# Optimization experiments

Hardware: AMD Instinct MI355X
Metric: run time of the kernel (lower is better)

Reference implementation:

```python
import jax, jax.numpy as jnp
import numpy as np

GRID = 128  # voxel grid extent
N_PTS = 100000


def _hash(c):
    c = c.astype(np.int64) + 16  # shift so offset-perturbed coords stay non-negative
    return (c[:, 0] * 512 + c[:, 1]) * 512 + c[:, 2]


def _offsets(vals):
    v = np.asarray(vals)
    return np.stack(np.meshgrid(v, v, v, indexing='ij'), axis=-1).reshape(-1, 3)


def _build_kmap(cin, cout, offsets):
    # For each kernel offset o, find pairs (in_idx, out_idx) with coord_in == coord_out + o.
    ki = _hash(cin)
    order = np.argsort(ki)
    ks = ki[order]
    ins, outs = [], []
    for o in offsets:
        q = _hash(cout + o[None, :])
        pos = np.searchsorted(ks, q)
        pc = np.clip(pos, 0, len(ks) - 1)
        found = ks[pc] == q
        ins.append(order[pc[found]])
        outs.append(np.nonzero(found)[0])
    K = len(offsets)
    P = max(1, max(len(a) for a in ins))
    in_idx = np.full((K, P), len(cin), np.int32)   # pad -> zero row of padded feats
    out_idx = np.full((K, P), len(cout), np.int32)  # pad -> dummy output row
    for k in range(K):
        in_idx[k, :len(ins[k])] = ins[k]
        out_idx[k, :len(outs[k])] = outs[k]
    return in_idx, out_idx


def _conv(x, W, in_idx, out_idx, n_out):
    # Minkowski sparse conv: per kernel offset, gather -> matmul -> scatter-add.
    xp = jnp.concatenate([x, jnp.zeros((1, x.shape[1]), x.dtype)], axis=0)
    out0 = jnp.zeros((n_out + 1, W.shape[-1]), x.dtype)

    def step(acc, kio):
        Wk, ik, ok = kio
        return acc.at[ok].add(xp[ik] @ Wk), None

    out, _ = jax.lax.scan(step, out0, (W, in_idx, out_idx))
    return out[:n_out]


def _bn(x, gamma, beta, eps=1e-5):
    # training-mode batch norm over the point dimension (biased variance)
    m = jnp.mean(x, axis=0)
    v = jnp.mean((x - m) ** 2, axis=0)
    return (x - m) * jax.lax.rsqrt(v + eps) * gamma + beta


def _forward(feats, W0, g0, b0,
             Ws1, gs1, bs1, Wa1, ga1, ba1, Wb1, gb1, bb1,
             Ws2, gs2, bs2, Wa2, ga2, ba2, Wb2, gb2, bb2, Wd2, gd2, bd2,
             Ws3, gs3, bs3, Wa3, ga3, ba3, Wb3, gb3, bb3, Wd3, gd3, bd3,
             c1, c2, c3,
             im0, om0, ims1, oms1, imb1, omb1, ims2, oms2, imb2, omb2,
             ims3, oms3, imb3, omb3):
    relu = jax.nn.relu
    n0, n1, n2, n3 = feats.shape[0], c1.shape[0], c2.shape[0], c3.shape[0]
    # stem: 5x5x5 conv + BN + ReLU (output coords == input coords)
    x = relu(_bn(_conv(feats, W0, im0, om0, n0), g0, b0))
    # level 1: stride-2 conv + BN + ReLU, then BasicBlock 64->64 (identity residual)
    x = relu(_bn(_conv(x, Ws1, ims1, oms1, n1), gs1, bs1))
    h = relu(_bn(_conv(x, Wa1, imb1, omb1, n1), ga1, ba1))
    h = _bn(_conv(h, Wb1, imb1, omb1, n1), gb1, bb1)
    y1 = relu(h + x)
    # level 2: stride-2 conv, then BasicBlock 64->128 (1x1 conv + BN residual)
    x = relu(_bn(_conv(y1, Ws2, ims2, oms2, n2), gs2, bs2))
    res = _bn(x @ Wd2, gd2, bd2)
    h = relu(_bn(_conv(x, Wa2, imb2, omb2, n2), ga2, ba2))
    h = _bn(_conv(h, Wb2, imb2, omb2, n2), gb2, bb2)
    y2 = relu(h + res)
    # level 3: stride-2 conv, then BasicBlock 128->256 (1x1 conv + BN residual)
    x = relu(_bn(_conv(y2, Ws3, ims3, oms3, n3), gs3, bs3))
    res = _bn(x @ Wd3, gd3, bd3)
    h = relu(_bn(_conv(x, Wa3, imb3, omb3, n3), ga3, ba3))
    h = _bn(_conv(h, Wb3, imb3, omb3, n3), gb3, bb3)
    y3 = relu(h + res)
    return (y1, y2, y3)


def setup_inputs() -> dict:
    rng = np.random.default_rng(0)
    c0 = np.unique(rng.integers(0, GRID, size=(N_PTS, 3)), axis=0).astype(np.int32)
    c1 = np.unique(c0 // 2 * 2, axis=0)
    c2 = np.unique(c1 // 4 * 4, axis=0)
    c3 = np.unique(c2 // 8 * 8, axis=0)
    im0, om0 = _build_kmap(c0, c0, _offsets([-2, -1, 0, 1, 2]))  # conv0 k=5, ts=1
    ims1, oms1 = _build_kmap(c0, c1, _offsets([0, 1]))           # stride-2, ts_in=1
    imb1, omb1 = _build_kmap(c1, c1, _offsets([-2, 0, 2]))       # k=3 at ts=2
    ims2, oms2 = _build_kmap(c1, c2, _offsets([0, 2]))
    imb2, omb2 = _build_kmap(c2, c2, _offsets([-4, 0, 4]))       # k=3 at ts=4
    ims3, oms3 = _build_kmap(c2, c3, _offsets([0, 4]))
    imb3, omb3 = _build_kmap(c3, c3, _offsets([-8, 0, 8]))       # k=3 at ts=8
    keys = iter(jax.random.split(jax.random.key(0), 16))

    def kai3(K, ci, co):  # kaiming_normal fan_out for [K, Cin, Cout] sparse kernels
        return jax.random.normal(next(keys), (K, ci, co), jnp.float32) * np.float32(np.sqrt(2.0 / (K * co)))

    def kai2(ci, co):
        return jax.random.normal(next(keys), (ci, co), jnp.float32) * np.float32(np.sqrt(2.0 / co))

    ones = lambda c: jnp.ones((c,), jnp.float32)
    zeros = lambda c: jnp.zeros((c,), jnp.float32)
    feats = jax.random.normal(next(keys), (c0.shape[0], 1), jnp.float32)
    return dict(
        feats=feats,
        W0=kai3(125, 1, 64), g0=ones(64), b0=zeros(64),
        Ws1=kai3(8, 64, 64), gs1=ones(64), bs1=zeros(64),
        Wa1=kai3(27, 64, 64), ga1=ones(64), ba1=zeros(64),
        Wb1=kai3(27, 64, 64), gb1=ones(64), bb1=zeros(64),
        Ws2=kai3(8, 64, 64), gs2=ones(64), bs2=zeros(64),
        Wa2=kai3(27, 64, 128), ga2=ones(128), ba2=zeros(128),
        Wb2=kai3(27, 128, 128), gb2=ones(128), bb2=zeros(128),
        Wd2=kai2(64, 128), gd2=ones(128), bd2=zeros(128),
        Ws3=kai3(8, 128, 128), gs3=ones(128), bs3=zeros(128),
        Wa3=kai3(27, 128, 256), ga3=ones(256), ba3=zeros(256),
        Wb3=kai3(27, 256, 256), gb3=ones(256), bb3=zeros(256),
        Wd3=kai2(128, 256), gd3=ones(256), bd3=zeros(256),
        c1=jnp.asarray(c1), c2=jnp.asarray(c2), c3=jnp.asarray(c3),
        im0=jnp.asarray(im0), om0=jnp.asarray(om0),
        ims1=jnp.asarray(ims1), oms1=jnp.asarray(oms1),
        imb1=jnp.asarray(imb1), omb1=jnp.asarray(omb1),
        ims2=jnp.asarray(ims2), oms2=jnp.asarray(oms2),
        imb2=jnp.asarray(imb2), omb2=jnp.asarray(omb2),
        ims3=jnp.asarray(ims3), oms3=jnp.asarray(oms3),
        imb3=jnp.asarray(imb3), omb3=jnp.asarray(omb3),
    )


def reference(feats, W0, g0, b0,
              Ws1, gs1, bs1, Wa1, ga1, ba1, Wb1, gb1, bb1,
              Ws2, gs2, bs2, Wa2, ga2, ba2, Wb2, gb2, bb2, Wd2, gd2, bd2,
              Ws3, gs3, bs3, Wa3, ga3, ba3, Wb3, gb3, bb3, Wd3, gd3, bd3,
              c1, c2, c3,
              im0, om0, ims1, oms1, imb1, omb1, ims2, oms2, imb2, omb2,
              ims3, oms3, imb3, omb3):
    return _forward(feats, W0, g0, b0,
                    Ws1, gs1, bs1, Wa1, ga1, ba1, Wb1, gb1, bb1,
                    Ws2, gs2, bs2, Wa2, ga2, ba2, Wb2, gb2, bb2, Wd2, gd2, bd2,
                    Ws3, gs3, bs3, Wa3, ga3, ba3, Wb3, gb3, bb3, Wd3, gd3, bd3,
                    c1, c2, c3,
                    im0, om0, ims1, oms1, imb1, omb1, ims2, oms2, imb2, omb2,
                    ims3, oms3, imb3, omb3)
```

## Files before the change

kernel.cpp:

```cpp
#include <hip/hip_runtime.h>
#include <hip/hip_bf16.h>
#include <cstdint>
#include <cstddef>

typedef __attribute__((ext_vector_type(8))) short sh8;
typedef __attribute__((ext_vector_type(4))) short sh4;
typedef __attribute__((ext_vector_type(4))) int ix4;
typedef __attribute__((ext_vector_type(16))) float floatx16;
typedef unsigned short ushort_t;

__device__ __forceinline__ void glds16(const ushort_t* g, ushort_t* l) {
  __builtin_amdgcn_global_load_lds(
      (const __attribute__((address_space(1))) void*)g,
      (__attribute__((address_space(3))) void*)l, 16, 0, 0);
}

__device__ __forceinline__ ushort_t f2bf_bits(float f) {
  __hip_bfloat16 b = __float2bfloat16(f);
  return __builtin_bit_cast(unsigned short, b);
}

__global__ void build_ell_kernel(const int* __restrict__ in_idx,
                                 const int* __restrict__ out_idx,
                                 int K, int S, int P, int n_in, int n_out,
                                 int* __restrict__ ell) {
  int i = blockIdx.x * 256 + threadIdx.x;
  if (i >= K * P) return;
  int vin = in_idx[i];
  int vout = out_idx[i];
  if (vin < n_in && vout < n_out) {
    ell[(size_t)vout * S + (i / P)] = vin;
  }
}

__global__ void pack_u_kernel(const float* __restrict__ W,
                              __hip_bfloat16* __restrict__ Wp,
                              int K, int CSPLIT, int COUT, long total) {
  long i = (long)blockIdx.x * 256 + threadIdx.x;
  if (i >= total) return;
  int co = (int)(i % COUT);
  long t = i / COUT;
  int vch = (int)(t % 64);
  int vk = (int)(t / 64);
  int k = vk / CSPLIT;
  int ci = (vk % CSPLIT) * 64 + vch;
  int CIN = CSPLIT * 64;
  float v = (k < K) ? W[((long)k * CIN + ci) * COUT + co] : 0.f;
  Wp[(((long)vk * 8 + (vch >> 3)) * COUT + co) * 8 + (vch & 7)] =
      __float2bfloat16(v);
}

__global__ void pack_w0_kernel(const float* __restrict__ W,
                               __hip_bfloat16* __restrict__ Wp) {
  int i = blockIdx.x * 256 + threadIdx.x;
  if (i >= 128 * 64) return;
  int co = i & 63;
  int ki = i >> 6;
  float v = (ki < 125) ? W[ki * 64 + co] : 0.f;
  Wp[(((ki >> 4) * 64) + co) * 16 + (ki & 15)] = __float2bfloat16(v);
}

__global__ void f2bf_kernel(const float* __restrict__ x,
                            __hip_bfloat16* __restrict__ y, long n, long npad) {
  long i = (long)blockIdx.x * 256 + threadIdx.x;
  if (i >= npad) return;
  y[i] = __float2bfloat16(i < n ? x[i] : 0.f);
}

__global__ void reduce_parts_kernel(const float* __restrict__ part, int P,
                                    long total, float* __restrict__ out) {
  long i = (long)blockIdx.x * 256 + threadIdx.x;
  if (i >= total) return;
  float s = 0.f;
  for (int p = 0; p < P; ++p) s += part[(size_t)p * total + i];
  out[i] = s;
}

__global__ __launch_bounds__(256, 2) void conv0_mfma_kernel(
    const ushort_t* __restrict__ xpad, const ushort_t* __restrict__ Wp0,
    const int* __restrict__ ell, int n_out, float* __restrict__ out) {
  constexpr int STR = 152;
  __shared__ ushort_t xs[64 * STR];
  const int tid = threadIdx.x;
  const int lane = tid & 63;
  const int wv = tid >> 6;
  const int wm = wv & 1, wn = wv >> 1;
  const long m0 = (long)blockIdx.x * 64;
  const int row = tid >> 2;
  const int kk0 = (tid & 3) * 32;
  const long grow = m0 + row;

  if (grow < n_out) {
    const ix4* ep = (const ix4*)(ell + grow * 128 + kk0);
#pragma unroll
    for (int g = 0; g < 8; ++g) {
      ix4 e = ep[g];
      sh4 v;
#pragma unroll
      for (int j = 0; j < 4; ++j) {
        int ix = (e[j] < 0) ? n_out : e[j];
        v[j] = (short)xpad[ix];
      }
      *(sh4*)(&xs[row * STR + kk0 + g * 4]) = v;
    }
  } else {
    sh4 z = (sh4)(short)0;
#pragma unroll
    for (int g = 0; g < 8; ++g) *(sh4*)(&xs[row * STR + kk0 + g * 4]) = z;
  }
  __syncthreads();

  const int arow = wm * 32 + (lane & 31);
  const int koff = (lane >> 5) * 8;
  const int bcol = wn * 32 + (lane & 31);
  floatx16 acc = (floatx16)(0.0f);
#pragma unroll
  for (int kc = 0; kc < 8; ++kc) {
    sh8 a = *(const sh8*)(&xs[arow * STR + kc * 16 + koff]);
    sh8 b = *(const sh8*)(Wp0 + ((size_t)kc * 64 + bcol) * 16 + koff);
    acc = __builtin_amdgcn_mfma_f32_32x32x16_bf16(a, b, acc, 0, 0, 0);
  }
  const int lrow = (lane >> 5) * 4;
#pragma unroll
  for (int r = 0; r < 16; ++r) {
    long orow = m0 + wm * 32 + (r & 3) + 8 * (r >> 2) + lrow;
    if (orow < n_out) out[orow * 64 + bcol] = acc[r];
  }
}

template <int CSPLIT, int CT>
__global__ __launch_bounds__(CT * 4, CT == 128 ? 4 : 2) void conv_u_kernel(
    const ushort_t* __restrict__ xb, const ushort_t* __restrict__ Wp,
    const int* __restrict__ ell, int S, int KI, int KP, int kdense,
    int n_out, int n_in, int COfull, int MB, int KS, int CS,
    float* __restrict__ out) {
  constexpr int BLK = CT * 4;
  constexpr int NWN = CT / 32;
  constexpr int ASEG_PW = 16 / (BLK / 64);
  constexpr int BSEG_PW = (CT / 8) / (BLK / 64);
  constexpr int RW = CSPLIT * 64;
  __shared__ ushort_t Ab[2][128 * 64];
  __shared__ ushort_t Bb[2][8 * CT * 8];
  __shared__ int ells[128 * 28];
  const int tid = threadIdx.x;
  const int lane = tid & 63;
  const int wv = tid >> 6;
  const int wm = wv / NWN, wn = wv % NWN;

  const int total = MB * KS * CS;
  const int l = blockIdx.x;
  const int q = total >> 3, r8 = total & 7;
  const int xcd = l & 7, pos = l >> 3;
  const int lp = (xcd < r8) ? (xcd * (q + 1) + pos)
                            : (r8 * (q + 1) + (xcd - r8) * q + pos);
  const int mblk = lp / (KS * CS);
  const int rem = lp - mblk * (KS * CS);
  const int yk = rem / CS;
  const int zc = rem - yk * CS;
  const long m0 = (long)mblk * 128;
  const int colbase = zc * CT;

  for (int idx = tid; idx < 128 * S; idx += BLK) {
    int r = idx / S, k = idx - r * S;
    long grow = m0 + r;
    int v = -1;
    if (grow < n_out) {
      if (ell) v = ell[grow * (long)S + k];
      else if (k < kdense) v = (int)grow;
    }
    ells[idx] = (v < 0) ? n_in : v;
  }
  __syncthreads();

  const int i0 = yk * KP;
  int cnt = KI - i0;
  if (cnt > KP) cnt = KP;
  out += (size_t)yk * ((size_t)n_out * COfull);

  floatx16 acc0 = (floatx16)(0.0f);
  floatx16 acc1 = (floatx16)(0.0f);

  auto stage = [&](int vk, ushort_t* A, ushort_t* B) {
    const int sub = (CSPLIT == 1) ? 0 : (vk % CSPLIT);
    const int kq = (CSPLIT == 1) ? vk : (vk / CSPLIT);
#pragma unroll
    for (int i = 0; i < ASEG_PW; ++i) {
      const int s = wv * ASEG_PW + i;
      const int r = s * 8 + (lane >> 3);
      const int c = lane & 7;
      const int lc = c ^ (r & 7);
      const int e = ells[r * S + kq];
      glds16(xb + (size_t)e * RW + sub * 64 + lc * 8, A + s * 512 + lane * 8);
    }
    const ushort_t* wb = Wp + (size_t)vk * 8 * COfull * 8;
#pragma unroll
    for (int i = 0; i < BSEG_PW; ++i) {
      const int s = wv * BSEG_PW + i;
      int lc, co;
      if (CT == 128) { lc = s >> 1; co = (s & 1) * 64 + lane; }
      else           { lc = s;      co = lane; }
      glds16(wb + ((size_t)lc * COfull + colbase + co) * 8,
             B + s * 512 + lane * 8);
    }
  };
  auto compute = [&](const ushort_t* A, const ushort_t* B) {
    const int r0 = wm * 64 + (lane & 31);
    const int h = lane >> 5;
    const int co = wn * 32 + (lane & 31);
#pragma unroll
    for (int kc = 0; kc < 4; ++kc) {
      const int lc = kc * 2 + h;
      const int pc = lc ^ (r0 & 7);
      sh8 a0 = *(const sh8*)(A + r0 * 64 + pc * 8);
      sh8 a1 = *(const sh8*)(A + (r0 + 32) * 64 + pc * 8);
      sh8 b = *(const sh8*)(B + ((size_t)lc * CT + co) * 8);
      acc0 = __builtin_amdgcn_mfma_f32_32x32x16_bf16(a0, b, acc0, 0, 0, 0);
      acc1 = __builtin_amdgcn_mfma_f32_32x32x16_bf16(a1, b, acc1, 0, 0, 0);
    }
  };

  stage(i0, Ab[0], Bb[0]);

#define CONV_ITER(J, P)                                                        \
  if ((J) < cnt) {                                                             \
    __builtin_amdgcn_s_barrier();                                              \
    if ((J) + 1 < cnt) {                                                       \
      stage(i0 + (J) + 1, Ab[(P) ^ 1], Bb[(P) ^ 1]);                           \
      if constexpr (CT == 128)                                                 \
        asm volatile("s_waitcnt vmcnt(4)" ::: "memory");                       \
      else                                                                     \
        asm volatile("s_waitcnt vmcnt(6)" ::: "memory");                       \
    } else {                                                                   \
      asm volatile("s_waitcnt vmcnt(0)" ::: "memory");                         \
    }                                                                          \
    __builtin_amdgcn_s_barrier();                                              \
    __builtin_amdgcn_sched_barrier(0);                                         \
    compute(Ab[P], Bb[P]);                                                     \
  }

  for (int j = 0; j < cnt; j += 2) {
    CONV_ITER(j, 0)
    CONV_ITER(j + 1, 1)
  }
#undef CONV_ITER

  const int ccol = colbase + wn * 32 + (lane & 31);
  const int rb = wm * 64 + (lane >> 5) * 4;
#pragma unroll
  for (int rr = 0; rr < 16; ++rr) {
    long row = m0 + rb + (rr & 3) + 8 * (rr >> 2);
    if (row < n_out) out[row * COfull + ccol] = acc0[rr];
    long row1 = row + 32;
    if (row1 < n_out) out[row1 * COfull + ccol] = acc1[rr];
  }
}

template <int C>
__global__ void bn_reduce1_kernel(const float* __restrict__ x, int n,
                                  float* __restrict__ part) {
  constexpr int C4 = C / 4;
  constexpr int RL = 256 / C4;
  const int c4 = threadIdx.x % C4;
  const int rl = threadIdx.x / C4;
  float4 s = {0.f, 0.f, 0.f, 0.f}, ss = {0.f, 0.f, 0.f, 0.f};
  for (long row = (long)blockIdx.x * RL + rl; row < n;
       row += (long)gridDim.x * RL) {
    float4 v = *(const float4*)(x + row * C + c4 * 4);
    s.x += v.x; s.y += v.y; s.z += v.z; s.w += v.w;
    ss.x += v.x * v.x; ss.y += v.y * v.y; ss.z += v.z * v.z; ss.w += v.w * v.w;
  }
  __shared__ float4 sh[512];
  sh[threadIdx.x] = s;
  sh[256 + threadIdx.x] = ss;
  __syncthreads();
  if (rl == 0) {
#pragma unroll
    for (int j = 1; j < RL; ++j) {
      float4 a = sh[j * C4 + c4];
      float4 b = sh[256 + j * C4 + c4];
      s.x += a.x; s.y += a.y; s.z += a.z; s.w += a.w;
      ss.x += b.x; ss.y += b.y; ss.z += b.z; ss.w += b.w;
    }
    *(float4*)(part + (size_t)blockIdx.x * 2 * C + c4 * 4) = s;
    *(float4*)(part + (size_t)blockIdx.x * 2 * C + C + c4 * 4) = ss;
  }
}

template <int C>
__global__ void bn_reduce2_kernel(const float* __restrict__ part, int G,
                                  float* __restrict__ stats) {
  const int c = blockIdx.x;
  const int g = threadIdx.x;
  __shared__ float sh[512];
  float s = 0.f, ss = 0.f;
  if (g < G) {
    s = part[(size_t)g * 2 * C + c];
    ss = part[(size_t)g * 2 * C + C + c];
  }
  sh[g] = s;
  sh[256 + g] = ss;
  __syncthreads();
#pragma unroll
  for (int off = 128; off > 0; off >>= 1) {
    if (g < off) {
      sh[g] += sh[g + off];
      sh[256 + g] += sh[256 + g + off];
    }
    __syncthreads();
  }
  if (g == 0) {
    stats[c] = sh[0];
    stats[C + c] = sh[256];
  }
}

template <int C, bool RELU, bool RES, bool WF32>
__global__ void bn_apply_kernel(const float* __restrict__ x,
                                const float* __restrict__ stats,
                                const float* __restrict__ gamma,
                                const float* __restrict__ beta,
                                const float* __restrict__ res,
                                long total4, float inv_n,
                                float* __restrict__ out,
                                ushort_t* __restrict__ outb, long padEnd4) {
  constexpr int C4 = C / 4;
  for (long i = (long)blockIdx.x * 256 + threadIdx.x; i < padEnd4;
       i += (long)gridDim.x * 256) {
    if (i >= total4) {
      if (outb) *(ushort4*)(outb + i * 4) = (ushort4){0, 0, 0, 0};
      continue;
    }
    const int c4 = (int)(i % C4);
    float4 sum = *(const float4*)(stats + c4 * 4);
    float4 sq = *(const float4*)(stats + C + c4 * 4);
    float4 g4 = *(const float4*)(gamma + c4 * 4);
    float4 b4 = *(const float4*)(beta + c4 * 4);
    float4 v = *(const float4*)(x + i * 4);
    float4 r4 = {0.f, 0.f, 0.f, 0.f};
    if (RES) r4 = *(const float4*)(res + i * 4);
    float o[4];
#pragma unroll
    for (int j = 0; j < 4; ++j) {
      float m = ((const float*)&sum)[j] * inv_n;
      float var = ((const float*)&sq)[j] * inv_n - m * m;
      float sc = rsqrtf(var + 1e-5f) * ((const float*)&g4)[j];
      float val = (((const float*)&v)[j] - m) * sc + ((const float*)&b4)[j];
      if (RES) val += ((const float*)&r4)[j];
      if (RELU) val = fmaxf(val, 0.f);
      o[j] = val;
    }
    if (WF32) *(float4*)(out + i * 4) = (float4){o[0], o[1], o[2], o[3]};
    if (outb) {
      ushort4 w = {f2bf_bits(o[0]), f2bf_bits(o[1]), f2bf_bits(o[2]),
                   f2bf_bits(o[3])};
      *(ushort4*)(outb + i * 4) = w;
    }
  }
}


extern "C" void kernel_launch(void* const* d_in, const int* in_sizes, int n_in,
                              void* d_out, int out_size, void* d_ws,
                              size_t ws_size, hipStream_t stream) {
  const float* feats = (const float*)d_in[0];
  const float* W0  = (const float*)d_in[1];
  const float* g0  = (const float*)d_in[2];
  const float* b0  = (const float*)d_in[3];
  const float* Ws1 = (const float*)d_in[4];
  const float* gs1 = (const float*)d_in[5];
  const float* bs1 = (const float*)d_in[6];
  const float* Wa1 = (const float*)d_in[7];
  const float* ga1 = (const float*)d_in[8];
  const float* ba1 = (const float*)d_in[9];
  const float* Wb1 = (const float*)d_in[10];
  const float* gb1 = (const float*)d_in[11];
  const float* bb1 = (const float*)d_in[12];
  const float* Ws2 = (const float*)d_in[13];
  const float* gs2 = (const float*)d_in[14];
  const float* bs2 = (const float*)d_in[15];
  const float* Wa2 = (const float*)d_in[16];
  const float* ga2 = (const float*)d_in[17];
  const float* ba2 = (const float*)d_in[18];
  const float* Wb2 = (const float*)d_in[19];
  const float* gb2 = (const float*)d_in[20];
  const float* bb2 = (const float*)d_in[21];
  const float* Wd2 = (const float*)d_in[22];
  const float* gd2 = (const float*)d_in[23];
  const float* bd2 = (const float*)d_in[24];
  const float* Ws3 = (const float*)d_in[25];
  const float* gs3 = (const float*)d_in[26];
  const float* bs3 = (const float*)d_in[27];
  const float* Wa3 = (const float*)d_in[28];
  const float* ga3 = (const float*)d_in[29];
  const float* ba3 = (const float*)d_in[30];
  const float* Wb3 = (const float*)d_in[31];
  const float* gb3 = (const float*)d_in[32];
  const float* bb3 = (const float*)d_in[33];
  const float* Wd3 = (const float*)d_in[34];
  const float* gd3 = (const float*)d_in[35];
  const float* bd3 = (const float*)d_in[36];
  const int* im0  = (const int*)d_in[40];
  const int* om0  = (const int*)d_in[41];
  const int* ims1 = (const int*)d_in[42];
  const int* oms1 = (const int*)d_in[43];
  const int* imb1 = (const int*)d_in[44];
  const int* omb1 = (const int*)d_in[45];
  const int* ims2 = (const int*)d_in[46];
  const int* oms2 = (const int*)d_in[47];
  const int* imb2 = (const int*)d_in[48];
  const int* omb2 = (const int*)d_in[49];
  const int* ims3 = (const int*)d_in[50];
  const int* oms3 = (const int*)d_in[51];
  const int* imb3 = (const int*)d_in[52];
  const int* omb3 = (const int*)d_in[53];

  const int n0 = in_sizes[0];
  const int n1 = in_sizes[37] / 3;
  const int n2 = in_sizes[38] / 3;
  const int n3 = in_sizes[39] / 3;
  const int P0  = in_sizes[40] / 125;
  const int Ps1 = in_sizes[42] / 8;
  const int Pb1 = in_sizes[44] / 27;
  const int Ps2 = in_sizes[46] / 8;
  const int Pb2 = in_sizes[48] / 27;
  const int Ps3 = in_sizes[50] / 8;
  const int Pb3 = in_sizes[52] / 27;

  char* w = (char*)d_ws;
  auto carve = [&](size_t bytes) {
    char* p = w;
    w += (bytes + 255) & ~(size_t)255;
    return p;
  };
  int* ellS = (int*)carve((size_t)n0 * 128 * sizeof(int));
  int* ellB = (int*)carve((size_t)n1 * 28 * sizeof(int));
  float* part = (float*)carve((size_t)256 * 512 * sizeof(float));
  float* stats = (float*)carve((size_t)512 * sizeof(float));
  size_t capE = (size_t)n0 * 64 + 512;
  float* buf1 = (float*)carve(capE * sizeof(float));
  float* buf2 = (float*)carve(capE * sizeof(float));
  float* buf3 = (float*)carve(capE * sizeof(float));
  __hip_bfloat16* bbA = (__hip_bfloat16*)carve(capE * 2);
  __hip_bfloat16* bbB = (__hip_bfloat16*)carve(capE * 2);
  __hip_bfloat16* bbC = (__hip_bfloat16*)carve(capE * 2);
  __hip_bfloat16* xfeat = (__hip_bfloat16*)carve(((size_t)n0 + 1) * 2);

  auto packu = [&](const float* W, int K, int cin, int cout) {
    int csplit = cin / 64;
    long tot = (long)K * csplit * 64 * cout;
    __hip_bfloat16* Wp = (__hip_bfloat16*)carve((size_t)tot * 2);
    pack_u_kernel<<<(int)((tot + 255) / 256), 256, 0, stream>>>(
        W, Wp, K, csplit, cout, tot);
    return Wp;
  };
  __hip_bfloat16* Wp0 = (__hip_bfloat16*)carve((size_t)128 * 64 * 2);
  pack_w0_kernel<<<32, 256, 0, stream>>>(W0, Wp0);
  __hip_bfloat16* Ps1p = packu(Ws1, 8, 64, 64);
  __hip_bfloat16* Pa1p = packu(Wa1, 27, 64, 64);
  __hip_bfloat16* Pb1p = packu(Wb1, 27, 64, 64);
  __hip_bfloat16* Ps2p = packu(Ws2, 8, 64, 64);
  __hip_bfloat16* Pd2p = packu(Wd2, 1, 64, 128);
  __hip_bfloat16* Pa2p = packu(Wa2, 27, 64, 128);
  __hip_bfloat16* Pb2p = packu(Wb2, 27, 128, 128);
  __hip_bfloat16* Ps3p = packu(Ws3, 8, 128, 128);
  __hip_bfloat16* Pd3p = packu(Wd3, 1, 128, 256);
  __hip_bfloat16* Pa3p = packu(Wa3, 27, 128, 256);
  __hip_bfloat16* Pb3p = packu(Wb3, 27, 256, 256);

  size_t used = (size_t)(w - (char*)d_ws);
  float* pbuf = (float*)w;
  size_t pcap = (ws_size > used) ? (ws_size - used) / sizeof(float) : 0;

  f2bf_kernel<<<(int)((n0 + 256) / 256), 256, 0, stream>>>(feats, xfeat, n0,
                                                           n0 + 1);

  auto buildEll = [&](int* ellbuf, const int* im, const int* om, int K, int S,
                      int P, int nin, int nout) {
    hipMemsetAsync(ellbuf, 0xFF, (size_t)nout * S * sizeof(int), stream);
    int tot = K * P;
    build_ell_kernel<<<(tot + 255) / 256, 256, 0, stream>>>(im, om, K, S, P,
                                                            nin, nout, ellbuf);
  };

  auto convu = [&](const __hip_bfloat16* xb, const __hip_bfloat16* Wp,
                   const int* ellp, int S, int K, int kdense, int nout,
                   int nin, int cin, int cout, float* outp) {
    int csplit = cin / 64;
    int KIv = K * csplit;
    int CT = (cout >= 128) ? 128 : 64;
    int cs = cout / CT;
    int mb = (nout + 127) / 128;
    int tiles = mb * cs;
    int ks = 1;
    if (tiles < 512 && KIv > 1) {
      ks = (512 + tiles - 1) / tiles;
      if (ks > 8) ks = 8;
      if (ks > KIv) ks = KIv;
      size_t need = (size_t)nout * cout;
      int fit = need ? (int)(pcap / need) : 1;
      if (ks > fit) ks = fit;
      if (ks < 1) ks = 1;
    }
    int KP = (KIv + ks - 1) / ks;
    int ksE = (KIv + KP - 1) / KP;
    float* tgt = (ksE > 1) ? pbuf : outp;
    int gridx = mb * ksE * cs;
#define CU_CASE(CSV, CTV)                                                      \
  else if (csplit == CSV && CT == CTV) {                                       \
    conv_u_kernel<CSV, CTV><<<gridx, CTV * 4, 0, stream>>>(                    \
        (const ushort_t*)xb, (const ushort_t*)Wp, ellp, S, KIv, KP, kdense,    \
        nout, nin, cout, mb, ksE, cs, tgt);                                    \
  }
    if (false) {}
    CU_CASE(1, 64)
    CU_CASE(1, 128)
    CU_CASE(2, 128)
    CU_CASE(4, 128)
#undef CU_CASE
    if (ksE > 1) {
      long total = (long)nout * cout;
      reduce_parts_kernel<<<(int)((total + 255) / 256), 256, 0, stream>>>(
          pbuf, ksE, total, outp);
    }
  };

  auto bn = [&](const float* x, int n, int C, const float* gamma,
                const float* beta, const float* res, bool relu, float* outp,
                __hip_bfloat16* outb) {
    const int G = 256;
    float invn = 1.0f / (float)n;
    long total4 = (long)n * C / 4;
    long padEnd4 = outb ? (total4 + C / 4) : total4;
    int agrid = (int)((padEnd4 + 255) / 256);
    if (agrid > 2048) agrid = 2048;
    ushort_t* outbu = (ushort_t*)outb;
#define BN_CASE(CC)                                                            \
  else if (C == CC) {                                                          \
    bn_reduce1_kernel<CC><<<G, 256, 0, stream>>>(x, n, part);                  \
    bn_reduce2_kernel<CC><<<CC, 256, 0, stream>>>(part, G, stats);             \
    if (res && relu)                                                           \
      bn_apply_kernel<CC, true, true, true><<<agrid, 256, 0, stream>>>(        \
          x, stats, gamma, beta, res, total4, invn, outp, outbu, padEnd4);     \
    else if (relu && outp)                                                     \
      bn_apply_kernel<CC, true, false, true><<<agrid, 256, 0, stream>>>(       \
          x, stats, gamma, beta, nullptr, total4, invn, outp, outbu,           \
          padEnd4);                                                            \
    else if (relu)                                                             \
      bn_apply_kernel<CC, true, false, false><<<agrid, 256, 0, stream>>>(      \
          x, stats, gamma, beta, nullptr, total4, invn, nullptr, outbu,        \
          padEnd4);                                                            \
    else                                                                       \
      bn_apply_kernel<CC, false, false, true><<<agrid, 256, 0, stream>>>(      \
          x, stats, gamma, beta, nullptr, total4, invn, outp, outbu,           \
          padEnd4);                                                            \
  }
    if (false) {}
    BN_CASE(64)
    BN_CASE(128)
    BN_CASE(256)
#undef BN_CASE
  };

  float* y1 = (float*)d_out;
  float* y2 = y1 + (size_t)n1 * 64;
  float* y3 = y2 + (size_t)n2 * 128;

  buildEll(ellS, im0, om0, 125, 128, P0, n0, n0);
  conv0_mfma_kernel<<<(n0 + 63) / 64, 256, 0, stream>>>(
      (const ushort_t*)xfeat, (const ushort_t*)Wp0, ellS, n0, buf1);
  bn(buf1, n0, 64, g0, b0, nullptr, true, nullptr, bbA);

  buildEll(ellS, ims1, oms1, 8, 8, Ps1, n0, n1);
  convu(bbA, Ps1p, ellS, 8, 8, 0, n1, n0, 64, 64, buf2);
  bn(buf2, n1, 64, gs1, bs1, nullptr, true, buf2, bbB);
  buildEll(ellB, imb1, omb1, 27, 28, Pb1, n1, n1);
  convu(bbB, Pa1p, ellB, 28, 27, 0, n1, n1, 64, 64, buf3);
  bn(buf3, n1, 64, ga1, ba1, nullptr, true, nullptr, bbC);
  convu(bbC, Pb1p, ellB, 28, 27, 0, n1, n1, 64, 64, buf1);
  bn(buf1, n1, 64, gb1, bb1, buf2, true, y1, bbA);

  buildEll(ellS, ims2, oms2, 8, 8, Ps2, n1, n2);
  convu(bbA, Ps2p, ellS, 8, 8, 0, n2, n1, 64, 64, buf3);
  bn(buf3, n2, 64, gs2, bs2, nullptr, true, nullptr, bbB);
  convu(bbB, Pd2p, nullptr, 1, 1, 1, n2, n2, 64, 128, buf1);
  bn(buf1, n2, 128, gd2, bd2, nullptr, false, buf1, nullptr);
  buildEll(ellB, imb2, omb2, 27, 28, Pb2, n2, n2);
  convu(bbB, Pa2p, ellB, 28, 27, 0, n2, n2, 64, 128, buf2);
  bn(buf2, n2, 128, ga2, ba2, nullptr, true, nullptr, bbC);
  convu(bbC, Pb2p, ellB, 28, 27, 0, n2, n2, 128, 128, buf3);
  bn(buf3, n2, 128, gb2, bb2, buf1, true, y2, bbA);

  buildEll(ellS, ims3, oms3, 8, 8, Ps3, n2, n3);
  convu(bbA, Ps3p, ellS, 8, 8, 0, n3, n2, 128, 128, buf2);
  bn(buf2, n3, 128, gs3, bs3, nullptr, true, nullptr, bbB);
  convu(bbB, Pd3p, nullptr, 1, 1, 1, n3, n3, 128, 256, buf1);
  bn(buf1, n3, 256, gd3, bd3, nullptr, false, buf1, nullptr);
  buildEll(ellB, imb3, omb3, 27, 28, Pb3, n3, n3);
  convu(bbB, Pa3p, ellB, 28, 27, 0, n3, n3, 128, 256, buf3);
  bn(buf3, n3, 256, ga3, ba3, nullptr, true, nullptr, bbC);
  convu(bbC, Pb3p, ellB, 28, 27, 0, n3, n3, 256, 256, buf2);
  bn(buf2, n3, 256, gb3, bb3, buf1, true, y3, nullptr);
}
```

Baseline: 708.9 us.

## Prefetch ELL indices into registers instead of staging full table in LDS

The conv kernel no longer copies the block's whole 128xS ELL index table into shared memory before the main loop. Instead, each lane loads only the indices it needs one or two steps ahead into registers, and the gather path is specialised at compile time on whether an ELL table exists. This removes a serial prologue load plus a __syncthreads, and frees LDS so the CT=64 variant's launch bounds can go from 2 to 3 blocks per CU. The cost is extra in-flight global loads per iteration, which forces a looser vmcnt wait, plus more register pressure.

```diff
diff --git a/kernel.cpp b/kernel.cpp
--- a/kernel.cpp
+++ b/kernel.cpp
@@ -128,8 +128,8 @@
   }
 }
 
-template <int CSPLIT, int CT>
-__global__ __launch_bounds__(CT * 4, CT == 128 ? 4 : 2) void conv_u_kernel(
+template <int CSPLIT, int CT, bool HASELL>
+__global__ __launch_bounds__(CT * 4, CT == 128 ? 4 : 3) void conv_u_kernel(
     const ushort_t* __restrict__ xb, const ushort_t* __restrict__ Wp,
     const int* __restrict__ ell, int S, int KI, int KP, int kdense,
     int n_out, int n_in, int COfull, int MB, int KS, int CS,
@@ -141,7 +141,6 @@
   constexpr int RW = CSPLIT * 64;
   __shared__ ushort_t Ab[2][128 * 64];
   __shared__ ushort_t Bb[2][8 * CT * 8];
-  __shared__ int ells[128 * 28];
   const int tid = threadIdx.x;
   const int lane = tid & 63;
   const int wv = tid >> 6;
@@ -160,18 +159,6 @@
   const long m0 = (long)mblk * 128;
   const int colbase = zc * CT;
 
-  for (int idx = tid; idx < 128 * S; idx += BLK) {
-    int r = idx / S, k = idx - r * S;
-    long grow = m0 + r;
-    int v = -1;
-    if (grow < n_out) {
-      if (ell) v = ell[grow * (long)S + k];
-      else if (k < kdense) v = (int)grow;
-    }
-    ells[idx] = (v < 0) ? n_in : v;
-  }
-  __syncthreads();
-
   const int i0 = yk * KP;
   int cnt = KI - i0;
   if (cnt > KP) cnt = KP;
@@ -180,16 +167,35 @@
   floatx16 acc0 = (floatx16)(0.0f);
   floatx16 acc1 = (floatx16)(0.0f);
 
-  auto stage = [&](int vk, ushort_t* A, ushort_t* B) {
+  auto loadEll = [&](int vk, int (&e)[ASEG_PW]) {
+    if constexpr (HASELL) {
+      const int kq = (CSPLIT == 1) ? vk : (vk / CSPLIT);
+#pragma unroll
+      for (int i = 0; i < ASEG_PW; ++i) {
+        const int s = wv * ASEG_PW + i;
+        const int r = s * 8 + (lane >> 3);
+        long grow = m0 + r;
+        long gc = grow < (long)(n_out - 1) ? grow : (long)(n_out - 1);
+        e[i] = ell[gc * (long)S + kq];
+      }
+    }
+  };
+
+  auto stage = [&](int vk, ushort_t* A, ushort_t* B, int (&eRaw)[ASEG_PW]) {
     const int sub = (CSPLIT == 1) ? 0 : (vk % CSPLIT);
     const int kq = (CSPLIT == 1) ? vk : (vk / CSPLIT);
 #pragma unroll
     for (int i = 0; i < ASEG_PW; ++i) {
       const int s = wv * ASEG_PW + i;
       const int r = s * 8 + (lane >> 3);
+      const long grow = m0 + r;
+      int v;
+      if constexpr (HASELL) v = eRaw[i];
+      else v = (kq < kdense) ? (int)grow : -1;
+      if (grow >= (long)n_out) v = -1;
+      const int e = (v < 0) ? n_in : v;
       const int c = lane & 7;
       const int lc = c ^ (r & 7);
-      const int e = ells[r * S + kq];
       glds16(xb + (size_t)e * RW + sub * 64 + lc * 8, A + s * 512 + lane * 8);
     }
     const ushort_t* wb = Wp + (size_t)vk * 8 * COfull * 8;
@@ -219,17 +225,25 @@
     }
   };
 
-  stage(i0, Ab[0], Bb[0]);
-
-#define CONV_ITER(J, P)                                                        \
+  constexpr int NWAIT = (ASEG_PW + BSEG_PW) + (HASELL ? ASEG_PW : 0);
+
+  int eE[ASEG_PW] = {}, eO[ASEG_PW] = {};
+  loadEll(i0, eE);
+  stage(i0, Ab[0], Bb[0], eE);
+  if (cnt > 1) loadEll(i0 + 1, eO);
+
+#define CONV_ITER(J, P, SE, SO)                                                \
   if ((J) < cnt) {                                                             \
     __builtin_amdgcn_s_barrier();                                              \
     if ((J) + 1 < cnt) {                                                       \
-      stage(i0 + (J) + 1, Ab[(P) ^ 1], Bb[(P) ^ 1]);                           \
-      if constexpr (CT == 128)                                                 \
+      stage(i0 + (J) + 1, Ab[(P) ^ 1], Bb[(P) ^ 1], SO);                       \
+      if ((J) + 2 < cnt) loadEll(i0 + (J) + 2, SE);                            \
+      if constexpr (NWAIT == 4)                                                \
         asm volatile("s_waitcnt vmcnt(4)" ::: "memory");                       \
+      else if constexpr (NWAIT == 6)                                           \
+        asm volatile("s_waitcnt vmcnt(6)" ::: "memory");                       \
       else                                                                     \
-        asm volatile("s_waitcnt vmcnt(6)" ::: "memory");                       \
+        asm volatile("s_waitcnt vmcnt(10)" ::: "memory");                      \
     } else {                                                                   \
       asm volatile("s_waitcnt vmcnt(0)" ::: "memory");                         \
     }                                                                          \
@@ -239,8 +253,8 @@
   }
 
   for (int j = 0; j < cnt; j += 2) {
-    CONV_ITER(j, 0)
-    CONV_ITER(j + 1, 1)
+    CONV_ITER(j, 0, eE, eO)
+    CONV_ITER(j + 1, 1, eO, eE)
   }
 #undef CONV_ITER
 
@@ -507,9 +521,14 @@
     int gridx = mb * ksE * cs;
 #define CU_CASE(CSV, CTV)                                                      \
   else if (csplit == CSV && CT == CTV) {                                       \
-    conv_u_kernel<CSV, CTV><<<gridx, CTV * 4, 0, stream>>>(                    \
-        (const ushort_t*)xb, (const ushort_t*)Wp, ellp, S, KIv, KP, kdense,    \
-        nout, nin, cout, mb, ksE, cs, tgt);                                    \
+    if (ellp)                                                                  \
+      conv_u_kernel<CSV, CTV, true><<<gridx, CTV * 4, 0, stream>>>(            \
+          (const ushort_t*)xb, (const ushort_t*)Wp, ellp, S, KIv, KP, kdense,  \
+          nout, nin, cout, mb, ksE, cs, tgt);                                  \
+    else                                                                       \
+      conv_u_kernel<CSV, CTV, false><<<gridx, CTV * 4, 0, stream>>>(           \
+          (const ushort_t*)xb, (const ushort_t*)Wp, ellp, S, KIv, KP, kdense,  \
+          nout, nin, cout, mb, ksE, cs, tgt);                                  \
   }
     if (false) {}
     CU_CASE(1, 64)
```

Result: faster. 648.6 us (-8.5%).
